# Optimization experiments

Hardware: AMD Instinct MI355X
Metric: run time of the kernel (lower is better)

The kernel has to match this reference:

```python
import jax, jax.numpy as jnp
import numpy as np

B, S, D, H = 2, 2048, 1024, 16
DK = D // H
EPS = 1e-6


def _rotate_half(x):
    x1, x2 = x[..., : x.shape[-1] // 2], x[..., x.shape[-1] // 2 :]
    return jnp.concatenate((-x2, x1), axis=-1)


def _rmsnorm(x, w):
    norm = jax.lax.rsqrt(jnp.mean(x * x, axis=-1, keepdims=True) + EPS)
    return x * norm * w


def setup_inputs() -> dict:
    key = jax.random.key(0)
    ks = jax.random.split(key, 12)
    q = jax.random.normal(ks[0], (B, S, D), jnp.float32)
    k = jax.random.normal(ks[1], (B, S, D), jnp.float32)
    v = jax.random.normal(ks[2], (B, S, D), jnp.float32)
    # causal mask, broadcastable over [B,H,S,S]; 0 => masked
    mask = jnp.tril(jnp.ones((S, S), jnp.int32))[None, None]
    # standard rotary tables
    inv_freq = 1.0 / (10000.0 ** (np.arange(0, DK, 2, dtype=np.float32) / DK))
    t = np.arange(S, dtype=np.float32)
    freqs = np.outer(t, inv_freq)  # [S, DK/2]
    emb = np.concatenate([freqs, freqs], axis=-1)  # [S, DK]
    cos = jnp.asarray(np.cos(emb))[None, None]  # [1,1,S,DK]
    sin = jnp.asarray(np.sin(emb))[None, None]
    sc = 1.0 / np.sqrt(D)
    wq = jax.random.normal(ks[3], (D, D), jnp.float32) * sc
    wk = jax.random.normal(ks[4], (D, D), jnp.float32) * sc
    wv = jax.random.normal(ks[5], (D, D), jnp.float32) * sc
    wo = jax.random.normal(ks[6], (D, D), jnp.float32) * sc
    bq = jnp.zeros((D,), jnp.float32)
    bk = jnp.zeros((D,), jnp.float32)
    bv = jnp.zeros((D,), jnp.float32)
    bo = jnp.zeros((D,), jnp.float32)
    qn_w = jnp.ones((DK,), jnp.float32)
    kn_w = jnp.ones((DK,), jnp.float32)
    return dict(q=q, k=k, v=v, mask=mask, cos=cos, sin=sin,
                wq=wq, bq=bq, wk=wk, bk=bk, wv=wv, bv=bv, wo=wo, bo=bo,
                qn_w=qn_w, kn_w=kn_w)


def reference(q, k, v, mask, cos, sin, wq, bq, wk, bk, wv, bv, wo, bo, qn_w, kn_w):
    b = q.shape[0]
    # QKV projections (torch Linear: x @ W.T + b)
    query = q @ wq.T + bq
    key = k @ wk.T + bk
    value = v @ wv.T + bv
    # [B,S,D] -> [B,H,S,DK]
    query = query.reshape(b, -1, H, DK).transpose(0, 2, 1, 3)
    key = key.reshape(b, -1, H, DK).transpose(0, 2, 1, 3)
    value = value.reshape(b, -1, H, DK).transpose(0, 2, 1, 3)
    # per-head QK RMSNorm
    query = _rmsnorm(query, qn_w)
    key = _rmsnorm(key, kn_w)
    # RoPE
    query = query * cos + _rotate_half(query) * sin
    key = key * cos + _rotate_half(key) * sin
    # naive attention
    scores = jnp.einsum('bhqd,bhkd->bhqk', query, key) / np.sqrt(DK).astype(np.float32)
    scores = jnp.where(mask == 0, jnp.float32(-1e9), scores)
    weights = jax.nn.softmax(scores, axis=-1)
    x = jnp.einsum('bhqk,bhkd->bhqd', weights, value)
    x = x.transpose(0, 2, 1, 3).reshape(b, -1, H * DK)
    return x @ wo.T + bo
```

## Files before the change

kernel.cpp:

```cpp
#include <hip/hip_runtime.h>

#define B_ 2
#define S_ 2048
#define D_ 1024
#define H_ 16
#define DK_ 64

typedef __attribute__((ext_vector_type(8))) short vshort8;
typedef __attribute__((ext_vector_type(4))) float vfloat4;

static __device__ inline unsigned short f2bf(float f) {
    unsigned int x = __float_as_uint(f);
    x += 0x7fffu + ((x >> 16) & 1u);
    return (unsigned short)(x >> 16);
}
static __device__ inline unsigned short f2bf_fast(float f) {
    return (unsigned short)((__float_as_uint(f) + 0x8000u) >> 16);
}
static __device__ inline float bf2f(unsigned short u) {
    return __uint_as_float((unsigned int)u << 16);
}

typedef __attribute__((address_space(1))) const unsigned int as1_uint;
typedef __attribute__((address_space(3))) unsigned int as3_uint;
static __device__ inline void async16(const void* g, void* l) {
    __builtin_amdgcn_global_load_lds((as1_uint*)g, (as3_uint*)l, 16, 0, 0);
}

__global__ __launch_bounds__(256) void cast_bf16_kernel(
    const float* s0, const float* s1, const float* s2, const float* s3,
    unsigned short* d0, unsigned short* d1, unsigned short* d2, unsigned short* d3)
{
    int z = blockIdx.z;
    const float* s = (z == 0) ? s0 : (z == 1) ? s1 : (z == 2) ? s2 : s3;
    unsigned short* d = (z == 0) ? d0 : (z == 1) ? d1 : (z == 2) ? d2 : d3;
    int i = (blockIdx.x * 256 + threadIdx.x) * 8;
    float4 f0 = *(const float4*)(s + i);
    float4 f1 = *(const float4*)(s + i + 4);
    uint4 o;
    o.x = (unsigned int)f2bf(f0.x) | ((unsigned int)f2bf(f0.y) << 16);
    o.y = (unsigned int)f2bf(f0.z) | ((unsigned int)f2bf(f0.w) << 16);
    o.z = (unsigned int)f2bf(f1.x) | ((unsigned int)f2bf(f1.y) << 16);
    o.w = (unsigned int)f2bf(f1.z) | ((unsigned int)f2bf(f1.w) << 16);
    *(uint4*)(d + i) = o;
}

__global__ __launch_bounds__(256) void gemm_bt_kernel(
    const unsigned short* __restrict__ A0, const unsigned short* __restrict__ A1, const unsigned short* __restrict__ A2,
    const unsigned short* __restrict__ W0, const unsigned short* __restrict__ W1, const unsigned short* __restrict__ W2,
    const float* __restrict__ bb0, const float* __restrict__ bb1, const float* __restrict__ bb2,
    unsigned short* __restrict__ o0, unsigned short* __restrict__ o1, unsigned short* __restrict__ o2,
    float* __restrict__ of,
    const float* __restrict__ nw0, const float* __restrict__ nw1,
    const float* __restrict__ cosb, const float* __restrict__ sinb,
    int mode)
{
    __shared__ unsigned short As[128][32];
    __shared__ unsigned short Ws[128][32];

    const int z = blockIdx.z;
    const unsigned short* A    = (z == 0) ? A0 : (z == 1) ? A1 : A2;
    const unsigned short* Wt   = (z == 0) ? W0 : (z == 1) ? W1 : W2;
    const float* bias          = (z == 0) ? bb0 : (z == 1) ? bb1 : bb2;

    const int tid  = threadIdx.x;
    const int wave = tid >> 6;
    const int lane = tid & 63;
    const int l15  = lane & 15;
    const int quad = lane >> 4;
    const int wm   = wave >> 1;
    const int wn   = wave & 1;
    const int m0   = blockIdx.y * 128;
    const int n0   = blockIdx.x * 128;

    const int li  = lane >> 2;
    const int lj  = lane & 3;
    const int lcc = (lj ^ ((li >> 1) & 3)) * 8;
    const int c0  = wave * 2;

    const unsigned short* gA0 = A  + (long)(m0 + c0 * 16      + li) * D_ + lcc;
    const unsigned short* gA1 = A  + (long)(m0 + c0 * 16 + 16 + li) * D_ + lcc;
    const unsigned short* gW0 = Wt + (long)(n0 + c0 * 16      + li) * D_ + lcc;
    const unsigned short* gW1 = Wt + (long)(n0 + c0 * 16 + 16 + li) * D_ + lcc;
    unsigned short* lA0 = (unsigned short*)As + (c0    ) * 512 + lane * 8;
    unsigned short* lA1 = (unsigned short*)As + (c0 + 1) * 512 + lane * 8;
    unsigned short* lW0 = (unsigned short*)Ws + (c0    ) * 512 + lane * 8;
    unsigned short* lW1 = (unsigned short*)Ws + (c0 + 1) * 512 + lane * 8;

    vfloat4 acc[4][4];
    for (int rt = 0; rt < 4; rt++)
        for (int ct = 0; ct < 4; ct++) {
            vfloat4 zz = {0.f, 0.f, 0.f, 0.f};
            acc[rt][ct] = zz;
        }

    const int sw = (quad ^ ((l15 >> 1) & 3)) * 8;

    for (int k0 = 0; k0 < 1024; k0 += 32) {
        async16(gA0 + k0, lA0);
        async16(gA1 + k0, lA1);
        async16(gW0 + k0, lW0);
        async16(gW1 + k0, lW1);
        __syncthreads();

        vshort8 af[4], bf[4];
        for (int rt = 0; rt < 4; rt++)
            af[rt] = *(const vshort8*)&As[wm * 64 + rt * 16 + l15][sw];
        for (int ct = 0; ct < 4; ct++)
            bf[ct] = *(const vshort8*)&Ws[wn * 64 + ct * 16 + l15][sw];
        for (int rt = 0; rt < 4; rt++)
            for (int ct = 0; ct < 4; ct++)
                acc[rt][ct] = __builtin_amdgcn_mfma_f32_16x16x32_bf16(af[rt], bf[ct], acc[rt][ct], 0, 0, 0);
        __syncthreads();
    }

    if (mode == 0) {
        for (int rt = 0; rt < 4; rt++) {
            int row = m0 + wm * 64 + rt * 16 + quad * 4;
            for (int ct = 0; ct < 4; ct++) {
                int col = n0 + wn * 64 + ct * 16 + l15;
                float bvv = bias[col];
                for (int r = 0; r < 4; r++)
                    of[(long)(row + r) * D_ + col] = acc[rt][ct][r] + bvv;
            }
        }
    } else if (z == 2) {
        for (int rt = 0; rt < 4; rt++) {
            int row = m0 + wm * 64 + rt * 16 + quad * 4;
            for (int ct = 0; ct < 4; ct++) {
                int col = n0 + wn * 64 + ct * 16 + l15;
                float bvv = bias[col];
                for (int r = 0; r < 4; r++)
                    o2[(long)(row + r) * D_ + col] = f2bf(acc[rt][ct][r] + bvv);
            }
        }
    } else {
        const float* w      = (z == 0) ? nw0 : nw1;
        unsigned short* out = (z == 0) ? o0  : o1;
        const float sfac    = (z == 0) ? 0.18033688011112042f : 1.0f;
        const int h = blockIdx.x * 2 + wn;
        float wv4[4], bv4[4];
        for (int ct = 0; ct < 4; ct++) {
            int dk = ct * 16 + l15;
            wv4[ct] = w[dk];
            bv4[ct] = bias[n0 + wn * 64 + dk];
        }
        for (int rt = 0; rt < 4; rt++) {
            for (int r = 0; r < 4; r++) {
                int row = m0 + wm * 64 + rt * 16 + quad * 4 + r;
                int s = row & (S_ - 1);
                int b = row >> 11;
                float x0 = acc[rt][0][r] + bv4[0];
                float x1 = acc[rt][1][r] + bv4[1];
                float x2 = acc[rt][2][r] + bv4[2];
                float x3 = acc[rt][3][r] + bv4[3];
                float ss = (x0 * x0 + x1 * x1) + (x2 * x2 + x3 * x3);
                ss += __shfl_xor(ss, 1, 64);
                ss += __shfl_xor(ss, 2, 64);
                ss += __shfl_xor(ss, 4, 64);
                ss += __shfl_xor(ss, 8, 64);
                float rn = rsqrtf(ss * (1.0f / 64.0f) + 1e-6f);
                float n0v = x0 * rn * wv4[0];
                float n1v = x1 * rn * wv4[1];
                float n2v = x2 * rn * wv4[2];
                float n3v = x3 * rn * wv4[3];
                long csb = (long)s * DK_ + l15;
                float c0v = cosb[csb], c1v = cosb[csb + 16], c2v = cosb[csb + 32], c3v = cosb[csb + 48];
                float s0v = sinb[csb], s1v = sinb[csb + 16], s2v = sinb[csb + 32], s3v = sinb[csb + 48];
                float v0 = (n0v * c0v - n2v * s0v) * sfac;
                float v1 = (n1v * c1v - n3v * s1v) * sfac;
                float v2 = (n2v * c2v + n0v * s2v) * sfac;
                float v3 = (n3v * c3v + n1v * s3v) * sfac;
                long ob = ((long)(b * H_ + h) * S_ + s) * DK_ + l15;
                out[ob]      = f2bf(v0);
                out[ob + 16] = f2bf(v1);
                out[ob + 32] = f2bf(v2);
                out[ob + 48] = f2bf(v3);
            }
        }
    }
}

__global__ __launch_bounds__(256) void transpose_v_kernel(
    const unsigned short* __restrict__ X,
    unsigned short* __restrict__ Vt)
{
    __shared__ unsigned short T[64][72];
    int st = blockIdx.x, bh = blockIdx.y;
    int b = bh >> 4, h = bh & 15;
    int s0 = st * 64;

    for (int it = 0; it < 2; it++) {
        int idx = threadIdx.x + it * 256;
        int r = idx >> 3;
        int c = (idx & 7) * 8;
        *(uint4*)&T[r][c] = *(const uint4*)&X[(long)(b * S_ + s0 + r) * D_ + h * 64 + c];
    }
    __syncthreads();
    for (int it = 0; it < 2; it++) {
        int idx = threadIdx.x + it * 256;
        int dk = idx >> 3;
        int ss = (idx & 7) * 8;
        unsigned short pk[8];
        for (int j = 0; j < 8; j++) pk[j] = T[ss + j][dk];
        *(uint4*)&Vt[((long)(b * H_ + h) * DK_ + dk) * S_ + s0 + ss] = *(uint4*)pk;
    }
}

__global__ __launch_bounds__(256, 2) void attn_kernel(
    const unsigned short* __restrict__ Q,
    const unsigned short* __restrict__ K,
    const unsigned short* __restrict__ Vt,
    unsigned short* __restrict__ O)
{
    __shared__ unsigned short Kbuf[2][64 * 64];
    __shared__ unsigned short Vbuf[2][64 * 64];
    __shared__ unsigned short Pscr[4][2][16 * 72];

    const int tid  = threadIdx.x;
    const int wave = tid >> 6;
    const int lane = tid & 63;
    const int l15  = lane & 15;
    const int quad = lane >> 4;
    const int qa   = blockIdx.x;
    const int qb   = 31 - qa;
    const int bh   = blockIdx.y;
    const int b    = bh >> 4;
    const int h    = bh & 15;
    const long baseQ = (long)bh * S_ * DK_;
    const long baseV = (long)bh * DK_ * S_;
    const float FM = 13.0f;

    const int rowc  = lane >> 3;
    const int slotS = ((lane & 7) ^ rowc) * 8;
    const int cA    = wave * 2, cB = wave * 2 + 1;

    const unsigned short* gK0 = K  + baseQ + (long)(cA * 8 + rowc) * DK_ + slotS;
    const unsigned short* gK1 = K  + baseQ + (long)(cB * 8 + rowc) * DK_ + slotS;
    const unsigned short* gV0 = Vt + baseV + (long)(cA * 8 + rowc) * S_ + slotS;
    const unsigned short* gV1 = Vt + baseV + (long)(cB * 8 + rowc) * S_ + slotS;
    const int ldsOffA = cA * 512 + lane * 8;
    const int ldsOffB = cB * 512 + lane * 8;

    vshort8 bqA[2], bqB[2];
    {
        int qA = qa * 64 + wave * 16 + l15;
        int qB = qb * 64 + wave * 16 + l15;
        for (int kh = 0; kh < 2; kh++) {
            bqA[kh] = *(const vshort8*)&Q[baseQ + (long)qA * DK_ + kh * 32 + quad * 8];
            bqB[kh] = *(const vshort8*)&Q[baseQ + (long)qB * DK_ + kh * 32 + quad * 8];
        }
    }

    vfloat4 OaccA[4], OaccB[4];
    for (int dt = 0; dt < 4; dt++) {
        vfloat4 zz = {0.f, 0.f, 0.f, 0.f};
        OaccA[dt] = zz; OaccB[dt] = zz;
    }
    float rsA = 0.f, rsB = 0.f;

    unsigned short* PA = &Pscr[wave][0][0];
    unsigned short* PB = &Pscr[wave][1][0];

    const int nkt = qb + 1;

    async16(gK0, &Kbuf[0][ldsOffA]);
    async16(gK1, &Kbuf[0][ldsOffB]);
    async16(gV0, &Vbuf[0][ldsOffA]);
    async16(gV1, &Vbuf[0][ldsOffB]);
    __syncthreads();

    for (int t = 0; t < nkt; t++) {
        const int cur = t & 1;
        if (t + 1 < nkt) {
            const int nxt = cur ^ 1;
            const long ko = (long)(t + 1) * 64;
            async16(gK0 + ko * DK_, &Kbuf[nxt][ldsOffA]);
            async16(gK1 + ko * DK_, &Kbuf[nxt][ldsOffB]);
            async16(gV0 + ko,       &Vbuf[nxt][ldsOffA]);
            async16(gV1 + ko,       &Vbuf[nxt][ldsOffB]);
        }

        vshort8 ak[4][2];
        for (int ct = 0; ct < 4; ct++)
            for (int kh = 0; kh < 2; kh++) {
                int r = ct * 16 + l15;
                int sl = (kh * 4 + quad) ^ (l15 & 7);
                ak[ct][kh] = *(const vshort8*)&Kbuf[cur][r * 64 + sl * 8];
            }
        vshort8 av[4][2];
        for (int dt = 0; dt < 4; dt++)
            for (int kh = 0; kh < 2; kh++) {
                int r = dt * 16 + l15;
                int sl = (kh * 4 + quad) ^ (l15 & 7);
                av[dt][kh] = *(const vshort8*)&Vbuf[cur][r * 64 + sl * 8];
            }

        const int k0 = t * 64;
        const bool actA = (t <= qa);

        if (actA) {
            vfloat4 sc[4];
            for (int ct = 0; ct < 4; ct++) {
                vfloat4 a = {0.f, 0.f, 0.f, 0.f};
                a = __builtin_amdgcn_mfma_f32_16x16x32_bf16(ak[ct][0], bqA[0], a, 0, 0, 0);
                a = __builtin_amdgcn_mfma_f32_16x16x32_bf16(ak[ct][1], bqA[1], a, 0, 0, 0);
                sc[ct] = a;
            }
            if (t == qa) {
                int qg = qa * 64 + wave * 16 + l15;
                for (int ct = 0; ct < 4; ct++) {
                    int kvb = k0 + ct * 16 + quad * 4;
                    for (int r = 0; r < 4; r++)
                        if (kvb + r > qg) sc[ct][r] = -1e30f;
                }
            }
            for (int ct = 0; ct < 4; ct++) {
                float p0 = exp2f(sc[ct][0] - FM);
                float p1 = exp2f(sc[ct][1] - FM);
                float p2 = exp2f(sc[ct][2] - FM);
                float p3 = exp2f(sc[ct][3] - FM);
                rsA += (p0 + p1) + (p2 + p3);
                uint2 o;
                o.x = (unsigned int)f2bf_fast(p0) | ((unsigned int)f2bf_fast(p1) << 16);
                o.y = (unsigned int)f2bf_fast(p2) | ((unsigned int)f2bf_fast(p3) << 16);
                *(uint2*)&PA[l15 * 72 + ct * 16 + quad * 4] = o;
            }
            vshort8 bp[2];
            for (int kh = 0; kh < 2; kh++)
                bp[kh] = *(const vshort8*)&PA[l15 * 72 + kh * 32 + quad * 8];
            for (int dt = 0; dt < 4; dt++) {
                OaccA[dt] = __builtin_amdgcn_mfma_f32_16x16x32_bf16(av[dt][0], bp[0], OaccA[dt], 0, 0, 0);
                OaccA[dt] = __builtin_amdgcn_mfma_f32_16x16x32_bf16(av[dt][1], bp[1], OaccA[dt], 0, 0, 0);
            }
        }

        {
            vfloat4 sc[4];
            for (int ct = 0; ct < 4; ct++) {
                vfloat4 a = {0.f, 0.f, 0.f, 0.f};
                a = __builtin_amdgcn_mfma_f32_16x16x32_bf16(ak[ct][0], bqB[0], a, 0, 0, 0);
                a = __builtin_amdgcn_mfma_f32_16x16x32_bf16(ak[ct][1], bqB[1], a, 0, 0, 0);
                sc[ct] = a;
            }
            if (t == nkt - 1) {
                int qg = qb * 64 + wave * 16 + l15;
                for (int ct = 0; ct < 4; ct++) {
                    int kvb = k0 + ct * 16 + quad * 4;
                    for (int r = 0; r < 4; r++)
                        if (kvb + r > qg) sc[ct][r] = -1e30f;
                }
            }
            for (int ct = 0; ct < 4; ct++) {
                float p0 = exp2f(sc[ct][0] - FM);
                float p1 = exp2f(sc[ct][1] - FM);
                float p2 = exp2f(sc[ct][2] - FM);
                float p3 = exp2f(sc[ct][3] - FM);
                rsB += (p0 + p1) + (p2 + p3);
                uint2 o;
                o.x = (unsigned int)f2bf_fast(p0) | ((unsigned int)f2bf_fast(p1) << 16);
                o.y = (unsigned int)f2bf_fast(p2) | ((unsigned int)f2bf_fast(p3) << 16);
                *(uint2*)&PB[l15 * 72 + ct * 16 + quad * 4] = o;
            }
            vshort8 bp[2];
            for (int kh = 0; kh < 2; kh++)
                bp[kh] = *(const vshort8*)&PB[l15 * 72 + kh * 32 + quad * 8];
            for (int dt = 0; dt < 4; dt++) {
                OaccB[dt] = __builtin_amdgcn_mfma_f32_16x16x32_bf16(av[dt][0], bp[0], OaccB[dt], 0, 0, 0);
                OaccB[dt] = __builtin_amdgcn_mfma_f32_16x16x32_bf16(av[dt][1], bp[1], OaccB[dt], 0, 0, 0);
            }
        }

        __syncthreads();
    }

    rsA += __shfl_xor(rsA, 16, 64);
    rsA += __shfl_xor(rsA, 32, 64);
    rsB += __shfl_xor(rsB, 16, 64);
    rsB += __shfl_xor(rsB, 32, 64);

    {
        float inv = 1.0f / rsA;
        int qg = qa * 64 + wave * 16 + l15;
        long rowbase = (long)(b * S_ + qg) * D_ + h * 64;
        for (int dt = 0; dt < 4; dt++) {
            unsigned short pk[4];
            for (int r = 0; r < 4; r++) pk[r] = f2bf(OaccA[dt][r] * inv);
            uint2 o;
            o.x = (unsigned int)pk[0] | ((unsigned int)pk[1] << 16);
            o.y = (unsigned int)pk[2] | ((unsigned int)pk[3] << 16);
            *(uint2*)&O[rowbase + dt * 16 + quad * 4] = o;
        }
    }
    {
        float inv = 1.0f / rsB;
        int qg = qb * 64 + wave * 16 + l15;
        long rowbase = (long)(b * S_ + qg) * D_ + h * 64;
        for (int dt = 0; dt < 4; dt++) {
            unsigned short pk[4];
            for (int r = 0; r < 4; r++) pk[r] = f2bf(OaccB[dt][r] * inv);
            uint2 o;
            o.x = (unsigned int)pk[0] | ((unsigned int)pk[1] << 16);
            o.y = (unsigned int)pk[2] | ((unsigned int)pk[3] << 16);
            *(uint2*)&O[rowbase + dt * 16 + quad * 4] = o;
        }
    }
}

extern "C" void kernel_launch(void* const* d_in, const int* in_sizes, int n_in,
                              void* d_out, int out_size, void* d_ws, size_t ws_size,
                              hipStream_t stream) {
    const float* q    = (const float*)d_in[0];
    const float* k    = (const float*)d_in[1];
    const float* v    = (const float*)d_in[2];
    const float* cosb = (const float*)d_in[4];
    const float* sinb = (const float*)d_in[5];
    const float* wq   = (const float*)d_in[6];
    const float* bq   = (const float*)d_in[7];
    const float* wk   = (const float*)d_in[8];
    const float* bk   = (const float*)d_in[9];
    const float* wv   = (const float*)d_in[10];
    const float* bv   = (const float*)d_in[11];
    const float* wo   = (const float*)d_in[12];
    const float* bo   = (const float*)d_in[13];
    const float* qn_w = (const float*)d_in[14];
    const float* kn_w = (const float*)d_in[15];

    const long MB = 1024 * 1024;
    char* ws = (char*)d_ws;
    unsigned short* xq   = (unsigned short*)(ws + 0 * MB);
    unsigned short* xk   = (unsigned short*)(ws + 8 * MB);
    unsigned short* xv   = (unsigned short*)(ws + 16 * MB);
    unsigned short* wqb  = (unsigned short*)(ws + 24 * MB);
    unsigned short* wkb  = (unsigned short*)(ws + 26 * MB);
    unsigned short* wvb  = (unsigned short*)(ws + 28 * MB);
    unsigned short* wob  = (unsigned short*)(ws + 30 * MB);
    unsigned short* Qn   = (unsigned short*)(ws + 32 * MB);
    unsigned short* Kn   = (unsigned short*)(ws + 40 * MB);
    unsigned short* tmpv = (unsigned short*)(ws + 48 * MB);
    unsigned short* Vtb  = (unsigned short*)(ws + 56 * MB);
    unsigned short* Ob   = (unsigned short*)(ws + 64 * MB);

    dim3 blk(256);
    cast_bf16_kernel<<<dim3(2048, 1, 3), blk, 0, stream>>>(q, k, v, q, xq, xk, xv, xq);
    cast_bf16_kernel<<<dim3(512, 1, 4), blk, 0, stream>>>(wq, wk, wv, wo, wqb, wkb, wvb, wob);

    gemm_bt_kernel<<<dim3(8, 32, 3), blk, 0, stream>>>(
        xq, xk, xv, wqb, wkb, wvb, bq, bk, bv,
        Qn, Kn, tmpv, nullptr, qn_w, kn_w, cosb, sinb, 1);

    transpose_v_kernel<<<dim3(32, 32), blk, 0, stream>>>(tmpv, Vtb);

    attn_kernel<<<dim3(16, 32), blk, 0, stream>>>(Qn, Kn, Vtb, Ob);

    gemm_bt_kernel<<<dim3(8, 32, 1), blk, 0, stream>>>(
        Ob, Ob, Ob, wob, wob, wob, bo, bo, bo,
        nullptr, nullptr, nullptr, (float*)d_out, nullptr, nullptr, nullptr, nullptr, 0);
}
```

Baseline: 271.3 us.

## Double-buffer GEMM LDS tiles, swizzle block order, merge cast kernels

Double-buffers the GEMM shared-memory tiles so the async global-to-LDS loads for the next K step are issued before the MFMAs on the current step, hiding load latency and dropping one barrier per iteration. It also remaps block indices so that consecutive blocks share weight column tiles, for better L2 reuse, and merges the two fp32-to-bf16 cast launches into one. The cost is doubled LDS use, which may lower occupancy. There is also a possible hazard: the asynchronous LDS writes into the other buffer overlap reads with only one barrier per iteration.

```diff
diff --git a/kernel.cpp b/kernel.cpp
--- a/kernel.cpp
+++ b/kernel.cpp
@@ -27,22 +27,37 @@
     __builtin_amdgcn_global_load_lds((as1_uint*)g, (as3_uint*)l, 16, 0, 0);
 }
 
-__global__ __launch_bounds__(256) void cast_bf16_kernel(
-    const float* s0, const float* s1, const float* s2, const float* s3,
-    unsigned short* d0, unsigned short* d1, unsigned short* d2, unsigned short* d3)
+__global__ __launch_bounds__(256) void cast_all_kernel(
+    const float* __restrict__ q, const float* __restrict__ k, const float* __restrict__ v,
+    const float* __restrict__ wq, const float* __restrict__ wk,
+    const float* __restrict__ wv, const float* __restrict__ wo,
+    unsigned short* __restrict__ xq, unsigned short* __restrict__ xk, unsigned short* __restrict__ xv,
+    unsigned short* __restrict__ wqb, unsigned short* __restrict__ wkb,
+    unsigned short* __restrict__ wvb, unsigned short* __restrict__ wob)
 {
-    int z = blockIdx.z;
-    const float* s = (z == 0) ? s0 : (z == 1) ? s1 : (z == 2) ? s2 : s3;
-    unsigned short* d = (z == 0) ? d0 : (z == 1) ? d1 : (z == 2) ? d2 : d3;
-    int i = (blockIdx.x * 256 + threadIdx.x) * 8;
-    float4 f0 = *(const float4*)(s + i);
-    float4 f1 = *(const float4*)(s + i + 4);
+    long idx = ((long)blockIdx.x * 256 + threadIdx.x) * 8;
+    int t22 = (int)(idx >> 22);
+    const float* s;
+    unsigned short* d;
+    long off;
+    if (t22 < 3) {
+        s = (t22 == 0) ? q : (t22 == 1) ? k : v;
+        d = (t22 == 0) ? xq : (t22 == 1) ? xk : xv;
+        off = idx & ((1L << 22) - 1);
+    } else {
+        int w = (int)(idx >> 20) & 3;
+        s = (w == 0) ? wq : (w == 1) ? wk : (w == 2) ? wv : wo;
+        d = (w == 0) ? wqb : (w == 1) ? wkb : (w == 2) ? wvb : wob;
+        off = idx & ((1L << 20) - 1);
+    }
+    float4 f0 = *(const float4*)(s + off);
+    float4 f1 = *(const float4*)(s + off + 4);
     uint4 o;
     o.x = (unsigned int)f2bf(f0.x) | ((unsigned int)f2bf(f0.y) << 16);
     o.y = (unsigned int)f2bf(f0.z) | ((unsigned int)f2bf(f0.w) << 16);
     o.z = (unsigned int)f2bf(f1.x) | ((unsigned int)f2bf(f1.y) << 16);
     o.w = (unsigned int)f2bf(f1.z) | ((unsigned int)f2bf(f1.w) << 16);
-    *(uint4*)(d + i) = o;
+    *(uint4*)(d + off) = o;
 }
 
 __global__ __launch_bounds__(256) void gemm_bt_kernel(
@@ -55,8 +70,8 @@
     const float* __restrict__ cosb, const float* __restrict__ sinb,
     int mode)
 {
-    __shared__ unsigned short As[128][32];
-    __shared__ unsigned short Ws[128][32];
+    __shared__ unsigned short As[2][128 * 32];
+    __shared__ unsigned short Ws[2][128 * 32];
 
     const int z = blockIdx.z;
     const unsigned short* A    = (z == 0) ? A0 : (z == 1) ? A1 : A2;
@@ -70,8 +85,12 @@
     const int quad = lane >> 4;
     const int wm   = wave >> 1;
     const int wn   = wave & 1;
-    const int m0   = blockIdx.y * 128;
-    const int n0   = blockIdx.x * 128;
+
+    const int bid = blockIdx.y * 8 + blockIdx.x;
+    const int byS = (bid & 7) * 4 + ((bid >> 3) & 3);
+    const int bxS = bid >> 5;
+    const int m0  = byS * 128;
+    const int n0  = bxS * 128;
 
     const int li  = lane >> 2;
     const int lj  = lane & 3;
@@ -82,10 +101,8 @@
     const unsigned short* gA1 = A  + (long)(m0 + c0 * 16 + 16 + li) * D_ + lcc;
     const unsigned short* gW0 = Wt + (long)(n0 + c0 * 16      + li) * D_ + lcc;
     const unsigned short* gW1 = Wt + (long)(n0 + c0 * 16 + 16 + li) * D_ + lcc;
-    unsigned short* lA0 = (unsigned short*)As + (c0    ) * 512 + lane * 8;
-    unsigned short* lA1 = (unsigned short*)As + (c0 + 1) * 512 + lane * 8;
-    unsigned short* lW0 = (unsigned short*)Ws + (c0    ) * 512 + lane * 8;
-    unsigned short* lW1 = (unsigned short*)Ws + (c0 + 1) * 512 + lane * 8;
+    const int st0 = c0 * 512 + lane * 8;
+    const int st1 = st0 + 512;
 
     vfloat4 acc[4][4];
     for (int rt = 0; rt < 4; rt++)
@@ -96,21 +113,32 @@
 
     const int sw = (quad ^ ((l15 >> 1) & 3)) * 8;
 
-    for (int k0 = 0; k0 < 1024; k0 += 32) {
-        async16(gA0 + k0, lA0);
-        async16(gA1 + k0, lA1);
-        async16(gW0 + k0, lW0);
-        async16(gW1 + k0, lW1);
-        __syncthreads();
+    async16(gA0, &As[0][st0]);
+    async16(gA1, &As[0][st1]);
+    async16(gW0, &Ws[0][st0]);
+    async16(gW1, &Ws[0][st1]);
+    __syncthreads();
+
+    for (int t = 0; t < 32; t++) {
+        const int cur = t & 1;
+        if (t < 31) {
+            const int nxt = cur ^ 1;
+            const int kn  = (t + 1) * 32;
+            async16(gA0 + kn, &As[nxt][st0]);
+            async16(gA1 + kn, &As[nxt][st1]);
+            async16(gW0 + kn, &Ws[nxt][st0]);
+            async16(gW1 + kn, &Ws[nxt][st1]);
+        }
 
         vshort8 af[4], bf[4];
         for (int rt = 0; rt < 4; rt++)
-            af[rt] = *(const vshort8*)&As[wm * 64 + rt * 16 + l15][sw];
+            af[rt] = *(const vshort8*)&As[cur][(wm * 64 + rt * 16 + l15) * 32 + sw];
         for (int ct = 0; ct < 4; ct++)
-            bf[ct] = *(const vshort8*)&Ws[wn * 64 + ct * 16 + l15][sw];
+            bf[ct] = *(const vshort8*)&Ws[cur][(wn * 64 + ct * 16 + l15) * 32 + sw];
         for (int rt = 0; rt < 4; rt++)
             for (int ct = 0; ct < 4; ct++)
                 acc[rt][ct] = __builtin_amdgcn_mfma_f32_16x16x32_bf16(af[rt], bf[ct], acc[rt][ct], 0, 0, 0);
+
         __syncthreads();
     }
 
@@ -138,7 +166,7 @@
         const float* w      = (z == 0) ? nw0 : nw1;
         unsigned short* out = (z == 0) ? o0  : o1;
         const float sfac    = (z == 0) ? 0.18033688011112042f : 1.0f;
-        const int h = blockIdx.x * 2 + wn;
+        const int h = bxS * 2 + wn;
         float wv4[4], bv4[4];
         for (int ct = 0; ct < 4; ct++) {
             int dk = ct * 16 + l15;
@@ -442,8 +470,8 @@
     unsigned short* Ob   = (unsigned short*)(ws + 64 * MB);
 
     dim3 blk(256);
-    cast_bf16_kernel<<<dim3(2048, 1, 3), blk, 0, stream>>>(q, k, v, q, xq, xk, xv, xq);
-    cast_bf16_kernel<<<dim3(512, 1, 4), blk, 0, stream>>>(wq, wk, wv, wo, wqb, wkb, wvb, wob);
+    cast_all_kernel<<<dim3(8192), blk, 0, stream>>>(
+        q, k, v, wq, wk, wv, wo, xq, xk, xv, wqb, wkb, wvb, wob);
 
     gemm_bt_kernel<<<dim3(8, 32, 3), blk, 0, stream>>>(
         xq, xk, xv, wqb, wkb, wvb, bq, bk, bv,
```

Result: no change. 272.1 us (+0.3%).
